# Kernel tuning notes

Measured on AMD Instinct MI355X. Metric: run time of the kernel, lower is better.

The kernel has to match this reference:

```python
import jax, jax.numpy as jnp
import numpy as np

N = 33554432  # 2**25 activations, 128 MB fp32
K = 1024      # winners kept


def setup_inputs() -> dict:
    key = jax.random.key(0)
    inputs = jax.random.normal(key, (N,), dtype=jnp.float32)
    return {"inputs": inputs, "k": K}


def reference(inputs, k):
    # k-th largest value = threshold (original: tf.sort desc, take element k-1)
    topk_vals, _ = jax.lax.top_k(inputs, k)
    threshold = topk_vals[k - 1]
    # zero out everything strictly below the threshold
    return jnp.where(inputs < threshold, jnp.zeros_like(inputs), inputs)
```

## Files before the change

### kernel.cpp

```cpp
#include <hip/hip_runtime.h>
#include <stdint.h>


#define HIST_BINS 4096
#define CTRL_OFF  HIST_BINS
#define CAND_OFF  (HIST_BINS + 16)

__device__ __forceinline__ uint32_t f2key(float x) {
  uint32_t u = __float_as_uint(x);
  return (u & 0x80000000u) ? ~u : (u | 0x80000000u);
}
__device__ __forceinline__ float key2f(uint32_t k) {
  uint32_t u = (k & 0x80000000u) ? (k & 0x7fffffffu) : ~k;
  return __uint_as_float(u);
}

__global__ void k_hist(const float4* __restrict__ in, int n4, int ntail,
                       const float* __restrict__ in_s,
                       uint32_t* __restrict__ ghist) {
  __shared__ uint32_t lh[HIST_BINS];
  for (int i = threadIdx.x; i < HIST_BINS; i += blockDim.x) lh[i] = 0;
  __syncthreads();
  int stride = gridDim.x * blockDim.x;
  for (int i = blockIdx.x * blockDim.x + threadIdx.x; i < n4; i += stride) {
    float4 v = in[i];
    atomicAdd(&lh[f2key(v.x) >> 20], 1u);
    atomicAdd(&lh[f2key(v.y) >> 20], 1u);
    atomicAdd(&lh[f2key(v.z) >> 20], 1u);
    atomicAdd(&lh[f2key(v.w) >> 20], 1u);
  }
  if (blockIdx.x == 0 && (int)threadIdx.x < ntail)
    atomicAdd(&lh[f2key(in_s[n4 * 4 + threadIdx.x]) >> 20], 1u);
  __syncthreads();
  for (int i = threadIdx.x; i < HIST_BINS; i += blockDim.x) {
    uint32_t c = lh[i];
    if (c) atomicAdd(&ghist[i], c);
  }
}

__global__ void k_select_bucket(const uint32_t* __restrict__ gh,
                                const int* __restrict__ kptr,
                                uint32_t* __restrict__ ctrl) {
  __shared__ uint32_t chunk[256];
  const int CPT = HIST_BINS / 256;
  int t = threadIdx.x;
  uint32_t s = 0;
  for (int i = 0; i < CPT; i++) s += gh[t * CPT + i];
  chunk[t] = s;
  __syncthreads();
  if (t == 0) {
    uint32_t K = (uint32_t)kptr[0];
    uint32_t above = 0;
    int sel = 0;
    for (int c = 255; c >= 0; c--) {
      if (above + chunk[c] >= K) { sel = c; break; }
      above += chunk[c];
    }
    int bsel = sel * CPT;
    for (int b = sel * CPT + CPT - 1; b >= sel * CPT; b--) {
      uint32_t c = gh[b];
      if (above + c >= K) { bsel = b; break; }
      above += c;
    }
    ctrl[1] = (uint32_t)bsel;
    ctrl[2] = K - above;
  }
}

__global__ void k_gather(const float4* __restrict__ in, int n4, int ntail,
                         const float* __restrict__ in_s,
                         uint32_t* __restrict__ ctrl,
                         uint32_t* __restrict__ cands, uint32_t cap) {
  uint32_t sel = ctrl[1];
  int stride = gridDim.x * blockDim.x;
  for (int i = blockIdx.x * blockDim.x + threadIdx.x; i < n4; i += stride) {
    float4 v = in[i];
    uint32_t k0 = f2key(v.x), k1 = f2key(v.y), k2 = f2key(v.z), k3 = f2key(v.w);
    if ((k0 >> 20) == sel) { uint32_t p = atomicAdd(&ctrl[0], 1u); if (p < cap) cands[p] = k0; }
    if ((k1 >> 20) == sel) { uint32_t p = atomicAdd(&ctrl[0], 1u); if (p < cap) cands[p] = k1; }
    if ((k2 >> 20) == sel) { uint32_t p = atomicAdd(&ctrl[0], 1u); if (p < cap) cands[p] = k2; }
    if ((k3 >> 20) == sel) { uint32_t p = atomicAdd(&ctrl[0], 1u); if (p < cap) cands[p] = k3; }
  }
  if (blockIdx.x == 0 && (int)threadIdx.x < ntail) {
    uint32_t kk = f2key(in_s[n4 * 4 + threadIdx.x]);
    if ((kk >> 20) == sel) { uint32_t p = atomicAdd(&ctrl[0], 1u); if (p < cap) cands[p] = kk; }
  }
}

__global__ void __launch_bounds__(1024) k_final(uint32_t* __restrict__ ctrl,
                                                const uint32_t* __restrict__ cands,
                                                uint32_t cap) {
  __shared__ uint32_t sh[8192];
  __shared__ uint32_t red[16];
  __shared__ uint32_t s_p, s_want;
  int t = threadIdx.x;
  uint32_t n = ctrl[0]; if (n > cap) n = cap;
  bool useLds = (n <= 8192);
  if (useLds) for (uint32_t i = t; i < n; i += blockDim.x) sh[i] = cands[i];
  if (t == 0) { s_p = ctrl[1] << 20; s_want = ctrl[2]; }
  __syncthreads();
  uint32_t p = s_p, want = s_want;
  for (int bit = 19; bit >= 0; bit--) {
    uint32_t test = p | (1u << bit);
    uint32_t hi = test >> bit;
    uint32_t cnt = 0;
    for (uint32_t i = t; i < n; i += blockDim.x) {
      uint32_t kk = useLds ? sh[i] : cands[i];
      cnt += ((kk >> bit) == hi) ? 1u : 0u;
    }
    for (int off = 32; off; off >>= 1) cnt += __shfl_down((int)cnt, off);
    int wave = t >> 6, lane = t & 63;
    if (lane == 0) red[wave] = cnt;
    __syncthreads();
    if (t == 0) {
      uint32_t tot = 0;
      for (int w = 0; w < 16; w++) tot += red[w];
      if (tot >= want) p = test; else want -= tot;
      s_p = p; s_want = want;
    }
    __syncthreads();
    p = s_p; want = s_want;
  }
  if (t == 0) ctrl[3] = __float_as_uint(key2f(p));
}

__global__ void k_apply(const float4* __restrict__ in, float4* __restrict__ out,
                        int n4, int ntail,
                        const float* __restrict__ in_s, float* __restrict__ out_s,
                        const uint32_t* __restrict__ ctrl) {
  float thr = __uint_as_float(ctrl[3]);
  int stride = gridDim.x * blockDim.x;
  for (int i = blockIdx.x * blockDim.x + threadIdx.x; i < n4; i += stride) {
    float4 v = in[i];
    v.x = (v.x < thr) ? 0.0f : v.x;
    v.y = (v.y < thr) ? 0.0f : v.y;
    v.z = (v.z < thr) ? 0.0f : v.z;
    v.w = (v.w < thr) ? 0.0f : v.w;
    out[i] = v;
  }
  if (blockIdx.x == 0 && (int)threadIdx.x < ntail) {
    float x = in_s[n4 * 4 + threadIdx.x];
    out_s[n4 * 4 + threadIdx.x] = (x < thr) ? 0.0f : x;
  }
}

extern "C" void kernel_launch(void* const* d_in, const int* in_sizes, int n_in,
                              void* d_out, int out_size, void* d_ws, size_t ws_size,
                              hipStream_t stream) {
  const float* in = (const float*)d_in[0];
  const int* kptr = (const int*)d_in[1];
  float* out = (float*)d_out;
  int n = in_sizes[0];
  int n4 = n >> 2;
  int ntail = n & 3;

  uint32_t* ws = (uint32_t*)d_ws;
  uint32_t* ghist = ws;
  uint32_t* ctrl = ws + CTRL_OFF;
  uint32_t* cands = ws + CAND_OFF;
  uint32_t cap = 0;
  size_t ws_words = ws_size / 4;
  if (ws_words > CAND_OFF) cap = (uint32_t)(ws_words - CAND_OFF);

  hipMemsetAsync(d_ws, 0, (CAND_OFF) * sizeof(uint32_t), stream);

  k_hist<<<1024, 256, 0, stream>>>((const float4*)in, n4, ntail, in, ghist);
  k_select_bucket<<<1, 256, 0, stream>>>(ghist, kptr, ctrl);
  k_gather<<<1024, 256, 0, stream>>>((const float4*)in, n4, ntail, in, ctrl, cands, cap);
  k_final<<<1, 1024, 0, stream>>>(ctrl, cands, cap);
  k_apply<<<4096, 256, 0, stream>>>((const float4*)in, (float4*)out, n4, ntail,
                                    in, out, ctrl);
}
```

Baseline: 294.6 us.

## Fuse threshold apply into gather pass and patch boundary bucket in final kernel

The separate apply pass is merged into the gather pass. Elements in buckets above the selected one are written directly, elements in the boundary bucket are written as zero, and their keys and indices are recorded. The final kernel then writes back the boundary-bucket candidates that are at or above the exact threshold. This removes one full read of the 128 MB input, and the output stores are made nontemporal. In exchange the candidate buffer is halved to make room for the index array, and correctness depends on every boundary candidate fitting in the capacity.

```diff
diff --git a/kernel.cpp b/kernel.cpp
--- a/kernel.cpp
+++ b/kernel.cpp
@@ -67,36 +67,55 @@
   }
 }
 
-__global__ void k_gather(const float4* __restrict__ in, int n4, int ntail,
-                         const float* __restrict__ in_s,
-                         uint32_t* __restrict__ ctrl,
-                         uint32_t* __restrict__ cands, uint32_t cap) {
+__global__ void k_apply_gather(const float4* __restrict__ in,
+                               float4* __restrict__ out, int n4, int ntail,
+                               const float* __restrict__ in_s,
+                               float* __restrict__ out_s,
+                               uint32_t* __restrict__ ctrl,
+                               uint32_t* __restrict__ keys,
+                               uint32_t* __restrict__ idxs, uint32_t cap) {
   uint32_t sel = ctrl[1];
   int stride = gridDim.x * blockDim.x;
   for (int i = blockIdx.x * blockDim.x + threadIdx.x; i < n4; i += stride) {
     float4 v = in[i];
     uint32_t k0 = f2key(v.x), k1 = f2key(v.y), k2 = f2key(v.z), k3 = f2key(v.w);
-    if ((k0 >> 20) == sel) { uint32_t p = atomicAdd(&ctrl[0], 1u); if (p < cap) cands[p] = k0; }
-    if ((k1 >> 20) == sel) { uint32_t p = atomicAdd(&ctrl[0], 1u); if (p < cap) cands[p] = k1; }
-    if ((k2 >> 20) == sel) { uint32_t p = atomicAdd(&ctrl[0], 1u); if (p < cap) cands[p] = k2; }
-    if ((k3 >> 20) == sel) { uint32_t p = atomicAdd(&ctrl[0], 1u); if (p < cap) cands[p] = k3; }
+    uint32_t b0 = k0 >> 20, b1 = k1 >> 20, b2 = k2 >> 20, b3 = k3 >> 20;
+    float4 r;
+    r.x = (b0 > sel) ? v.x : 0.0f;
+    r.y = (b1 > sel) ? v.y : 0.0f;
+    r.z = (b2 > sel) ? v.z : 0.0f;
+    r.w = (b3 > sel) ? v.w : 0.0f;
+    if (b0 == sel) { uint32_t p = atomicAdd(&ctrl[0], 1u); if (p < cap) { keys[p] = k0; idxs[p] = 4u * i + 0u; } }
+    if (b1 == sel) { uint32_t p = atomicAdd(&ctrl[0], 1u); if (p < cap) { keys[p] = k1; idxs[p] = 4u * i + 1u; } }
+    if (b2 == sel) { uint32_t p = atomicAdd(&ctrl[0], 1u); if (p < cap) { keys[p] = k2; idxs[p] = 4u * i + 2u; } }
+    if (b3 == sel) { uint32_t p = atomicAdd(&ctrl[0], 1u); if (p < cap) { keys[p] = k3; idxs[p] = 4u * i + 3u; } }
+    __builtin_nontemporal_store(r.x, &((float*)&out[i])[0]);
+    __builtin_nontemporal_store(r.y, &((float*)&out[i])[1]);
+    __builtin_nontemporal_store(r.z, &((float*)&out[i])[2]);
+    __builtin_nontemporal_store(r.w, &((float*)&out[i])[3]);
   }
   if (blockIdx.x == 0 && (int)threadIdx.x < ntail) {
-    uint32_t kk = f2key(in_s[n4 * 4 + threadIdx.x]);
-    if ((kk >> 20) == sel) { uint32_t p = atomicAdd(&ctrl[0], 1u); if (p < cap) cands[p] = kk; }
+    int j = n4 * 4 + threadIdx.x;
+    float x = in_s[j];
+    uint32_t kk = f2key(x);
+    uint32_t bb = kk >> 20;
+    out_s[j] = (bb > sel) ? x : 0.0f;
+    if (bb == sel) { uint32_t p = atomicAdd(&ctrl[0], 1u); if (p < cap) { keys[p] = kk; idxs[p] = (uint32_t)j; } }
   }
 }
 
 __global__ void __launch_bounds__(1024) k_final(uint32_t* __restrict__ ctrl,
-                                                const uint32_t* __restrict__ cands,
-                                                uint32_t cap) {
+                                                const uint32_t* __restrict__ keys,
+                                                const uint32_t* __restrict__ idxs,
+                                                uint32_t cap,
+                                                float* __restrict__ out_s) {
   __shared__ uint32_t sh[8192];
   __shared__ uint32_t red[16];
   __shared__ uint32_t s_p, s_want;
   int t = threadIdx.x;
   uint32_t n = ctrl[0]; if (n > cap) n = cap;
   bool useLds = (n <= 8192);
-  if (useLds) for (uint32_t i = t; i < n; i += blockDim.x) sh[i] = cands[i];
+  if (useLds) for (uint32_t i = t; i < n; i += blockDim.x) sh[i] = keys[i];
   if (t == 0) { s_p = ctrl[1] << 20; s_want = ctrl[2]; }
   __syncthreads();
   uint32_t p = s_p, want = s_want;
@@ -105,7 +124,7 @@
     uint32_t hi = test >> bit;
     uint32_t cnt = 0;
     for (uint32_t i = t; i < n; i += blockDim.x) {
-      uint32_t kk = useLds ? sh[i] : cands[i];
+      uint32_t kk = useLds ? sh[i] : keys[i];
       cnt += ((kk >> bit) == hi) ? 1u : 0u;
     }
     for (int off = 32; off; off >>= 1) cnt += __shfl_down((int)cnt, off);
@@ -122,25 +141,9 @@
     p = s_p; want = s_want;
   }
   if (t == 0) ctrl[3] = __float_as_uint(key2f(p));
-}
-
-__global__ void k_apply(const float4* __restrict__ in, float4* __restrict__ out,
-                        int n4, int ntail,
-                        const float* __restrict__ in_s, float* __restrict__ out_s,
-                        const uint32_t* __restrict__ ctrl) {
-  float thr = __uint_as_float(ctrl[3]);
-  int stride = gridDim.x * blockDim.x;
-  for (int i = blockIdx.x * blockDim.x + threadIdx.x; i < n4; i += stride) {
-    float4 v = in[i];
-    v.x = (v.x < thr) ? 0.0f : v.x;
-    v.y = (v.y < thr) ? 0.0f : v.y;
-    v.z = (v.z < thr) ? 0.0f : v.z;
-    v.w = (v.w < thr) ? 0.0f : v.w;
-    out[i] = v;
-  }
-  if (blockIdx.x == 0 && (int)threadIdx.x < ntail) {
-    float x = in_s[n4 * 4 + threadIdx.x];
-    out_s[n4 * 4 + threadIdx.x] = (x < thr) ? 0.0f : x;
+  for (uint32_t i = t; i < n; i += blockDim.x) {
+    uint32_t kk = useLds ? sh[i] : keys[i];
+    if (kk >= p) out_s[idxs[i]] = key2f(kk);
   }
 }
 
@@ -157,17 +160,17 @@
   uint32_t* ws = (uint32_t*)d_ws;
   uint32_t* ghist = ws;
   uint32_t* ctrl = ws + CTRL_OFF;
-  uint32_t* cands = ws + CAND_OFF;
+  size_t ws_words = ws_size / 4;
   uint32_t cap = 0;
-  size_t ws_words = ws_size / 4;
-  if (ws_words > CAND_OFF) cap = (uint32_t)(ws_words - CAND_OFF);
+  if (ws_words > CAND_OFF + 2) cap = (uint32_t)((ws_words - CAND_OFF) / 2);
+  uint32_t* keys = ws + CAND_OFF;
+  uint32_t* idxs = keys + cap;
 
-  hipMemsetAsync(d_ws, 0, (CAND_OFF) * sizeof(uint32_t), stream);
+  hipMemsetAsync(d_ws, 0, CAND_OFF * sizeof(uint32_t), stream);
 
   k_hist<<<1024, 256, 0, stream>>>((const float4*)in, n4, ntail, in, ghist);
   k_select_bucket<<<1, 256, 0, stream>>>(ghist, kptr, ctrl);
-  k_gather<<<1024, 256, 0, stream>>>((const float4*)in, n4, ntail, in, ctrl, cands, cap);
-  k_final<<<1, 1024, 0, stream>>>(ctrl, cands, cap);
-  k_apply<<<4096, 256, 0, stream>>>((const float4*)in, (float4*)out, n4, ntail,
-                                    in, out, ctrl);
+  k_apply_gather<<<4096, 256, 0, stream>>>((const float4*)in, (float4*)out,
+                                           n4, ntail, in, out, ctrl, keys, idxs, cap);
+  k_final<<<1, 1024, 0, stream>>>(ctrl, keys, idxs, cap, out);
 }
```

Result: faster. 274.1 us (-7.0%).
